# Kernel tuning notes

Hardware: AMD Instinct MI355X
Metric: run time of the kernel (lower is better)

Reference implementation:

```python
import jax, jax.numpy as jnp
import numpy as np

D_MODEL = 512
N_HEADS = 8
D_HEAD = D_MODEL // N_HEADS  # 64


def setup_inputs() -> dict:
    key = jax.random.key(0)
    ks = jax.random.split(key, 9)
    S = 4096
    sc_qkv = 1.0 / np.sqrt(D_MODEL)
    x = jax.random.normal(ks[0], (S, D_MODEL), dtype=jnp.float32)
    # per-head projection weights, stacked over heads: [H, D_MODEL, D_HEAD]
    Wq = jax.random.normal(ks[1], (N_HEADS, D_MODEL, D_HEAD), dtype=jnp.float32) * sc_qkv
    Wk = jax.random.normal(ks[2], (N_HEADS, D_MODEL, D_HEAD), dtype=jnp.float32) * sc_qkv
    Wv = jax.random.normal(ks[3], (N_HEADS, D_MODEL, D_HEAD), dtype=jnp.float32) * sc_qkv
    bq = jax.random.normal(ks[4], (N_HEADS, D_HEAD), dtype=jnp.float32) * 0.01
    bk = jax.random.normal(ks[5], (N_HEADS, D_HEAD), dtype=jnp.float32) * 0.01
    bv = jax.random.normal(ks[6], (N_HEADS, D_HEAD), dtype=jnp.float32) * 0.01
    # output projection (nn.Linear(512,512)): weight [out,in], bias [out]
    Wo = jax.random.normal(ks[7], (D_MODEL, D_MODEL), dtype=jnp.float32) * sc_qkv
    bo = jax.random.normal(ks[8], (D_MODEL,), dtype=jnp.float32) * 0.01
    return {"x": x, "Wq": Wq, "Wk": Wk, "Wv": Wv, "bq": bq, "bk": bk, "bv": bv, "Wo": Wo, "bo": bo}


def reference(x, Wq, Wk, Wv, bq, bk, bv, Wo, bo):
    # x: [S, D_MODEL]; all heads batched in one einsum (replaces python loop)
    q = jnp.einsum('sd,hdk->hsk', x, Wq) + bq[:, None, :]  # [H,S,Dh]
    k = jnp.einsum('sd,hdk->hsk', x, Wk) + bk[:, None, :]
    v = jnp.einsum('sd,hdk->hsk', x, Wv) + bv[:, None, :]
    scale = 1.0 / jnp.sqrt(jnp.asarray(D_HEAD, dtype=q.dtype))
    scores = jnp.einsum('hsk,htk->hst', q, k) * scale  # [H,S,S]
    attn = jax.nn.softmax(scores, axis=-1)
    ctx = jnp.einsum('hst,htk->hsk', attn, v)  # [H,S,Dh]
    # concat heads along feature dim: [S, H*Dh] (head-major order matches torch.concat)
    S = x.shape[0]
    concat = jnp.transpose(ctx, (1, 0, 2)).reshape(S, N_HEADS * D_HEAD)
    # nn.Linear: y = x @ W^T + b
    return concat @ Wo.T + bo
```

## Files before the change

kernel.cpp:

```cpp
#include <hip/hip_runtime.h>

#define S 4096
#define DM 512
#define NH 8
#define DHD 64
#define KVSPLIT 2
#define KVLEN (S / KVSPLIT)
#define ALPHA 0.18033688011112042f

using short8 = __attribute__((ext_vector_type(8))) short;
using f32x4  = __attribute__((ext_vector_type(4))) float;
using f32x16 = __attribute__((ext_vector_type(16))) float;

__device__ __forceinline__ unsigned short f2bf(float f) {
  union { float f; unsigned int u; } v; v.f = f;
  unsigned int r = v.u + 0x7FFF + ((v.u >> 16) & 1);
  return (unsigned short)(r >> 16);
}

__device__ __forceinline__ float bf2f(unsigned short u) {
  union { unsigned int u; float f; } v; v.u = (unsigned)u << 16;
  return v.f;
}

__device__ __forceinline__ unsigned int cvt_pk_bf16(float a, float b) {
  unsigned int r;
  asm("v_cvt_pk_bf16_f32 %0, %1, %2" : "=v"(r) : "v"(a), "v"(b));
  return r;
}

__device__ __forceinline__ void permswap(unsigned int& d, unsigned int& s) {
  asm("v_permlane32_swap_b32 %0, %1" : "+v"(d), "+v"(s));
}

__device__ __forceinline__ void async16(void* lds, const void* g) {
  __builtin_amdgcn_global_load_lds((const __attribute__((address_space(1))) void*)g,
                                   (__attribute__((address_space(3))) void*)lds, 16, 0, 0);
}

#define NCVT ((S * DM + DM * DM) / 1024)
__global__ void prep(const float* __restrict__ x, unsigned short* __restrict__ xb,
                     const float* __restrict__ Wo, unsigned short* __restrict__ Wob,
                     const float* __restrict__ Wq, const float* __restrict__ Wk,
                     const float* __restrict__ Wv, unsigned short* __restrict__ Wcat) {
  __shared__ float T[64][68];
  const int tid = threadIdx.x;
  if (blockIdx.x < NCVT) {
    int i = (blockIdx.x * 256 + tid) * 4;
    const float* src; unsigned short* dst;
    if (i < S * DM) { src = x + i; dst = xb + i; }
    else { int j = i - S * DM; src = Wo + j; dst = Wob + j; }
    float4 v = *(const float4*)src;
    uint2 o;
    o.x = (unsigned)f2bf(v.x) | ((unsigned)f2bf(v.y) << 16);
    o.y = (unsigned)f2bf(v.z) | ((unsigned)f2bf(v.w) << 16);
    *(uint2*)dst = o;
    return;
  }
  const int bid = blockIdx.x - NCVT;
  const int d0 = (bid & 7) * 64, h = (bid >> 3) & 7, t = bid >> 6;
  const float* W = (t == 0 ? Wq : t == 1 ? Wk : Wv) + (size_t)h * DM * DHD;
#pragma unroll
  for (int i = 0; i < 4; ++i) {
    int c = i * 256 + tid;
    int r = c >> 4, u = c & 15;
    *(float4*)&T[r][u * 4] = *(const float4*)&W[(size_t)(d0 + r) * DHD + u * 4];
  }
  __syncthreads();
#pragma unroll
  for (int i = 0; i < 2; ++i) {
    int c = i * 256 + tid;
    int dh = c >> 3, u = c & 7;
    unsigned short tmp[8];
#pragma unroll
    for (int j = 0; j < 8; ++j) tmp[j] = f2bf(T[u * 8 + j][dh]);
    *(uint4*)&Wcat[((size_t)(t * 512) + h * 64 + dh) * DM + d0 + u * 8] = *(uint4*)tmp;
  }
}

template <int EPI>
__global__ void __launch_bounds__(256, 4)
gemm_bt(const unsigned short* __restrict__ A,
        const unsigned short* __restrict__ B,
        int K,
        const float* __restrict__ b0, const float* __restrict__ b1, const float* __restrict__ b2,
        unsigned short* __restrict__ Qb, unsigned short* __restrict__ Kb, unsigned short* __restrict__ Vtb,
        float* __restrict__ outp) {
  __shared__ unsigned short As[128 * 32];
  __shared__ unsigned short Bs[64 * 32];
  const int tid = threadIdx.x;
  const int wid = tid >> 6, lane = tid & 63;
  const int lo = lane & 15, hi = lane >> 4;
  const int wr = wid >> 1, wc = wid & 1;
  const int m0 = blockIdx.x * 128, n0 = blockIdx.y * 64;
  f32x4 acc[4][2] = {};
  for (int k0 = 0; k0 < K; k0 += 32) {
    __syncthreads();
#pragma unroll
    for (int i = 0; i < 2; ++i) {
      const int cb = (wid * 2 + i) * 64;
      const int c = cb + lane, r = c >> 2, u = c & 3;
      async16(&As[cb * 8], A + (size_t)(m0 + r) * K + k0 + u * 8);
    }
    {
      const int cb = wid * 64;
      const int c = cb + lane, r = c >> 2, u = c & 3;
      async16(&Bs[cb * 8], B + (size_t)(n0 + r) * K + k0 + u * 8);
    }
    __syncthreads();
    short8 af[4], bfr[2];
#pragma unroll
    for (int m = 0; m < 4; ++m) af[m] = *(const short8*)&As[(wr * 64 + m * 16 + lo) * 32 + hi * 8];
#pragma unroll
    for (int n = 0; n < 2; ++n) bfr[n] = *(const short8*)&Bs[(wc * 32 + n * 16 + lo) * 32 + hi * 8];
#pragma unroll
    for (int m = 0; m < 4; ++m)
#pragma unroll
      for (int n = 0; n < 2; ++n)
        acc[m][n] = __builtin_amdgcn_mfma_f32_16x16x32_bf16(af[m], bfr[n], acc[m][n], 0, 0, 0);
  }
#pragma unroll
  for (int mi = 0; mi < 4; ++mi)
#pragma unroll
    for (int ni = 0; ni < 2; ++ni) {
      const int n = n0 + wc * 32 + ni * 16 + lo;
      const int mbase = m0 + wr * 64 + mi * 16 + hi * 4;
      if (EPI == 0) {
        const int t = n >> 9, h = (n >> 6) & 7, dh = n & 63;
        const float bias = (t == 0 ? b0 : t == 1 ? b1 : b2)[h * 64 + dh];
        if (t == 2) {
          unsigned short tmp[4];
#pragma unroll
          for (int r = 0; r < 4; ++r) tmp[r] = f2bf(acc[mi][ni][r] + bias);
          *(uint2*)&Vtb[((size_t)h * DHD + dh) * S + mbase] = *(uint2*)tmp;
        } else {
          unsigned short* dst = (t == 0 ? Qb : Kb);
#pragma unroll
          for (int r = 0; r < 4; ++r) {
            float v = acc[mi][ni][r] + bias;
            if (t == 0) v *= ALPHA;
            dst[((size_t)h * S + mbase + r) * DHD + dh] = f2bf(v);
          }
        }
      } else {
#pragma unroll
        for (int r = 0; r < 4; ++r)
          outp[(size_t)(mbase + r) * DM + n] = acc[mi][ni][r] + b0[n];
      }
    }
}

__global__ void __launch_bounds__(256, 2)
attn_kernel(const unsigned short* __restrict__ Qb, const unsigned short* __restrict__ Kb,
            const unsigned short* __restrict__ Vtb, unsigned short* __restrict__ accP,
            float2* __restrict__ lmP) {
  __shared__ unsigned short Ks[2][64 * 64];
  __shared__ unsigned short Vs[2][64 * 64];
  const int tid = threadIdx.x;
  const int wid = tid >> 6, lane = tid & 63;
  const int l = lane & 31, b = lane >> 5;
  const int h = blockIdx.y, sp = blockIdx.z;
  const int q0 = blockIdx.x * 128;
  const int kvbase = sp * KVLEN;
  const unsigned short* Qh  = Qb  + (size_t)h * S * DHD;
  const unsigned short* Kh  = Kb  + (size_t)h * S * DHD;
  const unsigned short* Vth = Vtb + (size_t)h * DHD * S;
  const int qrow = q0 + wid * 32 + l;
  short8 qf[4];
#pragma unroll
  for (int ks = 0; ks < 4; ++ks)
    qf[ks] = *(const short8*)&Qh[(size_t)qrow * DHD + ks * 16 + b * 8];

  float m_r = -__builtin_inff(), l_r = 0.f;
  f32x16 acc[2] = {};

  auto stage = [&](int bu, int kv0) {
#pragma unroll
    for (int i = 0; i < 2; ++i) {
      const int cb = (wid * 2 + i) * 64;
      const int c = cb + lane;
      const int r = c >> 3, up = c & 7;
      const int u = up ^ (r & 7);
      async16(&Ks[bu][cb * 8], Kh  + (size_t)(kv0 + r) * DHD + u * 8);
      async16(&Vs[bu][cb * 8], Vth + (size_t)r * S + kv0 + u * 8);
    }
  };

  stage(0, kvbase);
  __syncthreads();
  int cur = 0;
  for (int kv0 = kvbase; kv0 < kvbase + KVLEN; kv0 += 64) {
    if (kv0 + 64 < kvbase + KVLEN) stage(cur ^ 1, kv0 + 64);
    f32x16 sc[2];
    __builtin_amdgcn_s_setprio(1);
#pragma unroll
    for (int t = 0; t < 2; ++t) {
      sc[t] = (f32x16)0.0f;
#pragma unroll
      for (int ks = 0; ks < 4; ++ks) {
        const int r = t * 32 + l;
        const int u = ks * 2 + b;
        const short8 kfr = *(const short8*)&Ks[cur][r * 64 + (u ^ (r & 7)) * 8];
        sc[t] = __builtin_amdgcn_mfma_f32_32x32x16_bf16(kfr, qf[ks], sc[t], 0, 0, 0);
      }
    }
    __builtin_amdgcn_s_setprio(0);
    float mx[16];
#pragma unroll
    for (int i = 0; i < 16; ++i) mx[i] = fmaxf(sc[0][i], sc[1][i]);
#pragma unroll
    for (int s2 = 8; s2 > 0; s2 >>= 1)
#pragma unroll
      for (int i = 0; i < 8; ++i) if (i < s2) mx[i] = fmaxf(mx[i], mx[i + s2]);
    float pm = mx[0];
    pm = fmaxf(pm, __shfl_xor(pm, 32));
    if (__any(pm > m_r + 8.f)) {
      const float mn = fmaxf(m_r, pm);
      const float sca = exp2f(m_r - mn);
      m_r = mn;
      l_r *= sca;
#pragma unroll
      for (int dt = 0; dt < 2; ++dt)
#pragma unroll
        for (int i = 0; i < 16; ++i) acc[dt][i] *= sca;
    }
#pragma unroll
    for (int t = 0; t < 2; ++t)
#pragma unroll
      for (int i = 0; i < 16; ++i) sc[t][i] = exp2f(sc[t][i] - m_r);
    float sm[16];
#pragma unroll
    for (int i = 0; i < 16; ++i) sm[i] = sc[0][i] + sc[1][i];
#pragma unroll
    for (int s2 = 8; s2 > 0; s2 >>= 1)
#pragma unroll
      for (int i = 0; i < 8; ++i) if (i < s2) sm[i] += sm[i + s2];
    float ps = sm[0];
    ps += __shfl_xor(ps, 32);
    l_r += ps;
    __builtin_amdgcn_s_setprio(1);
#pragma unroll
    for (int t = 0; t < 2; ++t) {
      unsigned int pk[8];
#pragma unroll
      for (int i = 0; i < 8; ++i) pk[i] = cvt_pk_bf16(sc[t][2 * i], sc[t][2 * i + 1]);
#pragma unroll
      for (int kse = 0; kse < 2; ++kse) {
        unsigned int a0 = pk[4 * kse + 0], a1 = pk[4 * kse + 1];
        unsigned int c0 = pk[4 * kse + 2], c1 = pk[4 * kse + 3];
        permswap(a0, c0);
        permswap(a1, c1);
        uint4 pw = make_uint4(a0, a1, c0, c1);
        const short8 pb = *(const short8*)&pw;
        const int ks = t * 2 + kse;
#pragma unroll
        for (int dt = 0; dt < 2; ++dt) {
          const int r2 = dt * 32 + l;
          const int u = ks * 2 + b;
          const short8 vf = *(const short8*)&Vs[cur][r2 * 64 + (u ^ (r2 & 7)) * 8];
          acc[dt] = __builtin_amdgcn_mfma_f32_32x32x16_bf16(vf, pb, acc[dt], 0, 0, 0);
        }
      }
    }
    __builtin_amdgcn_s_setprio(0);
    __syncthreads();
    cur ^= 1;
  }
  const size_t prow = (size_t)(sp * NH + h) * S + qrow;
#pragma unroll
  for (int dt = 0; dt < 2; ++dt)
#pragma unroll
    for (int qd = 0; qd < 4; ++qd) {
      unsigned int w0 = cvt_pk_bf16(acc[dt][4 * qd + 0], acc[dt][4 * qd + 1]);
      unsigned int w1 = cvt_pk_bf16(acc[dt][4 * qd + 2], acc[dt][4 * qd + 3]);
      *(uint2*)&accP[prow * 64 + dt * 32 + qd * 8 + b * 4] = make_uint2(w0, w1);
    }
  if (b == 0) lmP[prow] = make_float2(m_r, l_r);
}

__global__ void merge_kernel(const unsigned short* __restrict__ accP, const float2* __restrict__ lmP,
                             unsigned short* __restrict__ concat) {
  const int c = blockIdx.x * 256 + threadIdx.x;
  const int row = c >> 3;
  const int h = row >> 12, q = row & (S - 1);
  const int dh0 = (c & 7) * 8;
  const float2 lm0 = lmP[row];
  const float2 lm1 = lmP[NH * S + row];
  const float M = fmaxf(lm0.x, lm1.x);
  float w0 = exp2f(lm0.x - M), w1 = exp2f(lm1.x - M);
  const float inv = 1.f / (lm0.y * w0 + lm1.y * w1);
  w0 *= inv; w1 *= inv;
  const short8 v0 = *(const short8*)&accP[(size_t)row * 64 + dh0];
  const short8 v1 = *(const short8*)&accP[((size_t)NH * S + row) * 64 + dh0];
  unsigned short out[8];
#pragma unroll
  for (int j = 0; j < 8; ++j)
    out[j] = f2bf(bf2f((unsigned short)v0[j]) * w0 + bf2f((unsigned short)v1[j]) * w1);
  *(uint4*)&concat[(size_t)q * DM + h * DHD + dh0] = *(uint4*)out;
}

extern "C" void kernel_launch(void* const* d_in, const int* in_sizes, int n_in,
                              void* d_out, int out_size, void* d_ws, size_t ws_size,
                              hipStream_t stream) {
  const float* x  = (const float*)d_in[0];
  const float* Wq = (const float*)d_in[1];
  const float* Wk = (const float*)d_in[2];
  const float* Wv = (const float*)d_in[3];
  const float* bq = (const float*)d_in[4];
  const float* bk = (const float*)d_in[5];
  const float* bv = (const float*)d_in[6];
  const float* Wo = (const float*)d_in[7];
  const float* bo = (const float*)d_in[8];
  float* outp = (float*)d_out;
  char* ws = (char*)d_ws;
  unsigned short* Qbuf   = (unsigned short*)(ws + 0);
  unsigned short* Kbuf   = (unsigned short*)(ws + 4194304);
  unsigned short* Vtbuf  = (unsigned short*)(ws + 8388608);
  unsigned short* concat = (unsigned short*)(ws + 12582912);
  unsigned short* Wob    = (unsigned short*)(ws + 16777216);
  float2*         lmP    = (float2*)(ws + 17301504);
  unsigned short* xb     = (unsigned short*)(ws + 17825792);
  unsigned short* Wcat   = (unsigned short*)(ws + 22020096);
  unsigned short* accP   = (unsigned short*)(ws + 17825792);

  prep<<<NCVT + 192, 256, 0, stream>>>(x, xb, Wo, Wob, Wq, Wk, Wv, Wcat);
  gemm_bt<0><<<dim3(S / 128, 1536 / 64), 256, 0, stream>>>(xb, Wcat, DM, bq, bk, bv,
                                                           Qbuf, Kbuf, Vtbuf, nullptr);
  attn_kernel<<<dim3(S / 128, NH, KVSPLIT), 256, 0, stream>>>(Qbuf, Kbuf, Vtbuf, accP, lmP);
  merge_kernel<<<(NH * S * 8) / 256, 256, 0, stream>>>(accP, lmP, concat);
  gemm_bt<1><<<dim3(S / 128, DM / 64), 256, 0, stream>>>(concat, Wob, DM, bo, nullptr, nullptr,
                                                         nullptr, nullptr, nullptr, outp);
}
```

Baseline: 174.1 us.

## Increase attention KV split to four and retile output GEMM to 64x64

Makes the attention KV-split count a template parameter and picks 4 splits when the workspace is large enough, otherwise 2. The merge kernel is generalised to any number of splits. The output projection gets its own 64x64-tile GEMM so it launches more blocks, and attention occupancy is raised to 4 blocks per SM. The aim is better GPU fill in attention and the output GEMM, at the cost of more partial-result traffic and merge work.

Measured after the change: 164.3 us. 5.6% less time.

```diff
diff --git a/kernel.cpp b/kernel.cpp
--- a/kernel.cpp
+++ b/kernel.cpp
@@ -4,8 +4,6 @@
 #define DM 512
 #define NH 8
 #define DHD 64
-#define KVSPLIT 2
-#define KVLEN (S / KVSPLIT)
 #define ALPHA 0.18033688011112042f
 
 using short8 = __attribute__((ext_vector_type(8))) short;
@@ -78,14 +76,11 @@
   }
 }
 
-template <int EPI>
 __global__ void __launch_bounds__(256, 4)
-gemm_bt(const unsigned short* __restrict__ A,
-        const unsigned short* __restrict__ B,
-        int K,
-        const float* __restrict__ b0, const float* __restrict__ b1, const float* __restrict__ b2,
-        unsigned short* __restrict__ Qb, unsigned short* __restrict__ Kb, unsigned short* __restrict__ Vtb,
-        float* __restrict__ outp) {
+gemm_qkv(const unsigned short* __restrict__ A,
+         const unsigned short* __restrict__ B,
+         const float* __restrict__ b0, const float* __restrict__ b1, const float* __restrict__ b2,
+         unsigned short* __restrict__ Qb, unsigned short* __restrict__ Kb, unsigned short* __restrict__ Vtb) {
   __shared__ unsigned short As[128 * 32];
   __shared__ unsigned short Bs[64 * 32];
   const int tid = threadIdx.x;
@@ -94,18 +89,18 @@
   const int wr = wid >> 1, wc = wid & 1;
   const int m0 = blockIdx.x * 128, n0 = blockIdx.y * 64;
   f32x4 acc[4][2] = {};
-  for (int k0 = 0; k0 < K; k0 += 32) {
+  for (int k0 = 0; k0 < DM; k0 += 32) {
     __syncthreads();
 #pragma unroll
     for (int i = 0; i < 2; ++i) {
       const int cb = (wid * 2 + i) * 64;
       const int c = cb + lane, r = c >> 2, u = c & 3;
-      async16(&As[cb * 8], A + (size_t)(m0 + r) * K + k0 + u * 8);
+      async16(&As[cb * 8], A + (size_t)(m0 + r) * DM + k0 + u * 8);
     }
     {
       const int cb = wid * 64;
       const int c = cb + lane, r = c >> 2, u = c & 3;
-      async16(&Bs[cb * 8], B + (size_t)(n0 + r) * K + k0 + u * 8);
+      async16(&Bs[cb * 8], B + (size_t)(n0 + r) * DM + k0 + u * 8);
     }
     __syncthreads();
     short8 af[4], bfr[2];
@@ -125,35 +120,74 @@
     for (int ni = 0; ni < 2; ++ni) {
       const int n = n0 + wc * 32 + ni * 16 + lo;
       const int mbase = m0 + wr * 64 + mi * 16 + hi * 4;
-      if (EPI == 0) {
-        const int t = n >> 9, h = (n >> 6) & 7, dh = n & 63;
-        const float bias = (t == 0 ? b0 : t == 1 ? b1 : b2)[h * 64 + dh];
-        if (t == 2) {
-          unsigned short tmp[4];
-#pragma unroll
-          for (int r = 0; r < 4; ++r) tmp[r] = f2bf(acc[mi][ni][r] + bias);
-          *(uint2*)&Vtb[((size_t)h * DHD + dh) * S + mbase] = *(uint2*)tmp;
-        } else {
-          unsigned short* dst = (t == 0 ? Qb : Kb);
-#pragma unroll
-          for (int r = 0; r < 4; ++r) {
-            float v = acc[mi][ni][r] + bias;
-            if (t == 0) v *= ALPHA;
-            dst[((size_t)h * S + mbase + r) * DHD + dh] = f2bf(v);
-          }
+      const int t = n >> 9, h = (n >> 6) & 7, dh = n & 63;
+      const float bias = (t == 0 ? b0 : t == 1 ? b1 : b2)[h * 64 + dh];
+      if (t == 2) {
+        unsigned short tmp[4];
+#pragma unroll
+        for (int r = 0; r < 4; ++r) tmp[r] = f2bf(acc[mi][ni][r] + bias);
+        *(uint2*)&Vtb[((size_t)h * DHD + dh) * S + mbase] = *(uint2*)tmp;
+      } else {
+        unsigned short* dst = (t == 0 ? Qb : Kb);
+#pragma unroll
+        for (int r = 0; r < 4; ++r) {
+          float v = acc[mi][ni][r] + bias;
+          if (t == 0) v *= ALPHA;
+          dst[((size_t)h * S + mbase + r) * DHD + dh] = f2bf(v);
         }
-      } else {
-#pragma unroll
-        for (int r = 0; r < 4; ++r)
-          outp[(size_t)(mbase + r) * DM + n] = acc[mi][ni][r] + b0[n];
       }
     }
 }
 
-__global__ void __launch_bounds__(256, 2)
+__global__ void __launch_bounds__(256, 4)
+gemm_out(const unsigned short* __restrict__ A,
+         const unsigned short* __restrict__ B,
+         const float* __restrict__ bias, float* __restrict__ outp) {
+  __shared__ unsigned short As[64 * 32];
+  __shared__ unsigned short Bs[64 * 32];
+  const int tid = threadIdx.x;
+  const int wid = tid >> 6, lane = tid & 63;
+  const int lo = lane & 15, hi = lane >> 4;
+  const int wr = wid >> 1, wc = wid & 1;
+  const int m0 = blockIdx.x * 64, n0 = blockIdx.y * 64;
+  f32x4 acc[2][2] = {};
+  for (int k0 = 0; k0 < DM; k0 += 32) {
+    __syncthreads();
+    {
+      const int c = wid * 64 + lane, r = c >> 2, u = c & 3;
+      async16(&As[wid * 64 * 8], A + (size_t)(m0 + r) * DM + k0 + u * 8);
+      async16(&Bs[wid * 64 * 8], B + (size_t)(n0 + r) * DM + k0 + u * 8);
+    }
+    __syncthreads();
+    short8 af[2], bfr[2];
+#pragma unroll
+    for (int m = 0; m < 2; ++m) af[m] = *(const short8*)&As[(wr * 32 + m * 16 + lo) * 32 + hi * 8];
+#pragma unroll
+    for (int n = 0; n < 2; ++n) bfr[n] = *(const short8*)&Bs[(wc * 32 + n * 16 + lo) * 32 + hi * 8];
+#pragma unroll
+    for (int m = 0; m < 2; ++m)
+#pragma unroll
+      for (int n = 0; n < 2; ++n)
+        acc[m][n] = __builtin_amdgcn_mfma_f32_16x16x32_bf16(af[m], bfr[n], acc[m][n], 0, 0, 0);
+  }
+#pragma unroll
+  for (int mi = 0; mi < 2; ++mi)
+#pragma unroll
+    for (int ni = 0; ni < 2; ++ni) {
+      const int n = n0 + wc * 32 + ni * 16 + lo;
+      const int mbase = m0 + wr * 32 + mi * 16 + hi * 4;
+#pragma unroll
+      for (int r = 0; r < 4; ++r)
+        outp[(size_t)(mbase + r) * DM + n] = acc[mi][ni][r] + bias[n];
+    }
+}
+
+template <int NSPLIT>
+__global__ void __launch_bounds__(256, 4)
 attn_kernel(const unsigned short* __restrict__ Qb, const unsigned short* __restrict__ Kb,
             const unsigned short* __restrict__ Vtb, unsigned short* __restrict__ accP,
             float2* __restrict__ lmP) {
+  constexpr int KVLEN = S / NSPLIT;
   __shared__ unsigned short Ks[2][64 * 64];
   __shared__ unsigned short Vs[2][64 * 64];
   const int tid = threadIdx.x;
@@ -278,24 +312,31 @@
   if (b == 0) lmP[prow] = make_float2(m_r, l_r);
 }
 
+template <int NSPLIT>
 __global__ void merge_kernel(const unsigned short* __restrict__ accP, const float2* __restrict__ lmP,
                              unsigned short* __restrict__ concat) {
   const int c = blockIdx.x * 256 + threadIdx.x;
   const int row = c >> 3;
   const int h = row >> 12, q = row & (S - 1);
   const int dh0 = (c & 7) * 8;
-  const float2 lm0 = lmP[row];
-  const float2 lm1 = lmP[NH * S + row];
-  const float M = fmaxf(lm0.x, lm1.x);
-  float w0 = exp2f(lm0.x - M), w1 = exp2f(lm1.x - M);
-  const float inv = 1.f / (lm0.y * w0 + lm1.y * w1);
-  w0 *= inv; w1 *= inv;
-  const short8 v0 = *(const short8*)&accP[(size_t)row * 64 + dh0];
-  const short8 v1 = *(const short8*)&accP[((size_t)NH * S + row) * 64 + dh0];
+  float2 lm[NSPLIT];
+  float M = -__builtin_inff();
+#pragma unroll
+  for (int s = 0; s < NSPLIT; ++s) { lm[s] = lmP[(size_t)s * NH * S + row]; M = fmaxf(M, lm[s].x); }
+  float w[NSPLIT], denom = 0.f;
+#pragma unroll
+  for (int s = 0; s < NSPLIT; ++s) { w[s] = exp2f(lm[s].x - M); denom += lm[s].y * w[s]; }
+  const float inv = 1.f / denom;
+  float o[8] = {};
+#pragma unroll
+  for (int s = 0; s < NSPLIT; ++s) {
+    const short8 v = *(const short8*)&accP[((size_t)s * NH * S + row) * 64 + dh0];
+#pragma unroll
+    for (int j = 0; j < 8; ++j) o[j] += bf2f((unsigned short)v[j]) * w[s];
+  }
   unsigned short out[8];
 #pragma unroll
-  for (int j = 0; j < 8; ++j)
-    out[j] = f2bf(bf2f((unsigned short)v0[j]) * w0 + bf2f((unsigned short)v1[j]) * w1);
+  for (int j = 0; j < 8; ++j) out[j] = f2bf(o[j] * inv);
   *(uint4*)&concat[(size_t)q * DM + h * DHD + dh0] = *(uint4*)out;
 }
 
@@ -313,21 +354,26 @@
   const float* bo = (const float*)d_in[8];
   float* outp = (float*)d_out;
   char* ws = (char*)d_ws;
+  const int nsplit = (ws_size >= 35127296u) ? 4 : 2;
   unsigned short* Qbuf   = (unsigned short*)(ws + 0);
   unsigned short* Kbuf   = (unsigned short*)(ws + 4194304);
   unsigned short* Vtbuf  = (unsigned short*)(ws + 8388608);
   unsigned short* concat = (unsigned short*)(ws + 12582912);
   unsigned short* Wob    = (unsigned short*)(ws + 16777216);
   float2*         lmP    = (float2*)(ws + 17301504);
-  unsigned short* xb     = (unsigned short*)(ws + 17825792);
-  unsigned short* Wcat   = (unsigned short*)(ws + 22020096);
-  unsigned short* accP   = (unsigned short*)(ws + 17825792);
+  const size_t xb_off    = 17301504 + (size_t)nsplit * NH * S * sizeof(float2);
+  unsigned short* xb     = (unsigned short*)(ws + xb_off);
+  unsigned short* Wcat   = (unsigned short*)(ws + xb_off + 4194304);
+  unsigned short* accP   = (unsigned short*)(ws + xb_off);
 
   prep<<<NCVT + 192, 256, 0, stream>>>(x, xb, Wo, Wob, Wq, Wk, Wv, Wcat);
-  gemm_bt<0><<<dim3(S / 128, 1536 / 64), 256, 0, stream>>>(xb, Wcat, DM, bq, bk, bv,
-                                                           Qbuf, Kbuf, Vtbuf, nullptr);
-  attn_kernel<<<dim3(S / 128, NH, KVSPLIT), 256, 0, stream>>>(Qbuf, Kbuf, Vtbuf, accP, lmP);
-  merge_kernel<<<(NH * S * 8) / 256, 256, 0, stream>>>(accP, lmP, concat);
-  gemm_bt<1><<<dim3(S / 128, DM / 64), 256, 0, stream>>>(concat, Wob, DM, bo, nullptr, nullptr,
-                                                         nullptr, nullptr, nullptr, outp);
-}
+  gemm_qkv<<<dim3(S / 128, 1536 / 64), 256, 0, stream>>>(xb, Wcat, bq, bk, bv, Qbuf, Kbuf, Vtbuf);
+  if (nsplit == 4) {
+    attn_kernel<4><<<dim3(S / 128, NH, 4), 256, 0, stream>>>(Qbuf, Kbuf, Vtbuf, accP, lmP);
+    merge_kernel<4><<<(NH * S * 8) / 256, 256, 0, stream>>>(accP, lmP, concat);
+  } else {
+    attn_kernel<2><<<dim3(S / 128, NH, 2), 256, 0, stream>>>(Qbuf, Kbuf, Vtbuf, accP, lmP);
+    merge_kernel<2><<<(NH * S * 8) / 256, 256, 0, stream>>>(accP, lmP, concat);
+  }
+  gemm_out<<<dim3(S / 64, DM / 64), 256, 0, stream>>>(concat, Wob, bo, outp);
+}
```
